# Kernel tuning notes

Hardware: AMD Instinct MI355X
Metric: run time of the kernel (lower is better)

The kernel has to match this reference:

```python
import jax, jax.numpy as jnp
import numpy as np

CDIM = 256  # part_size for energy_pooling_mask


def setup_inputs() -> dict:
    key = jax.random.key(0)
    ks = jax.random.split(key, 6)
    B, T, IDIM, HDIM, ODIM = 8, 2048, 512, 2048, 512
    x = jax.random.normal(ks[0], (B, T, IDIM), dtype=jnp.float32)
    mask_prev = jax.random.randint(ks[1], (B, T, HDIM), 0, 2, dtype=jnp.int32)
    W_enc = jax.random.normal(ks[2], (HDIM, IDIM), dtype=jnp.float32) * 0.02
    b_enc = jax.random.normal(ks[3], (HDIM,), dtype=jnp.float32) * 0.02
    W_dec = jax.random.normal(ks[4], (ODIM, HDIM), dtype=jnp.float32) * 0.02
    b_dec = jax.random.normal(ks[5], (ODIM,), dtype=jnp.float32) * 0.02
    return {"x": x, "mask_prev": mask_prev, "W_enc": W_enc, "b_enc": b_enc,
            "W_dec": W_dec, "b_dec": b_dec}


def _energy_pooling_mask(h, part_size):
    # topk over channel (last) dim of h^2; share=True -> k = 2*part_size
    B, T, H = h.shape
    k2 = 2 * part_size
    _, idx = jax.lax.top_k(h * h, k2)            # [B, T, 2c] unique indices
    idx_f = idx.reshape(B * T, k2)
    rows = jnp.arange(B * T)[:, None]
    base = jnp.zeros((B * T, H), dtype=h.dtype)
    # sum of one-hots over unique indices == scatter-set of 1.0
    mask_share = base.at[rows, idx_f].set(1.0).reshape(B, T, H)
    mask_cur = base.at[rows, idx_f[:, :part_size]].set(1.0).reshape(B, T, H)
    return mask_cur, mask_share


def reference(x, mask_prev, W_enc, b_enc, W_dec, b_dec):
    # encoder: Linear(idim -> hdim)
    h = jnp.einsum('bti,hi->bth', x, W_enc) + b_enc
    # hidden_exclude_activation with mask_prev given:
    # h[mask_prev.bool()] = 0
    mp = mask_prev.astype(h.dtype)
    h = jnp.where(mp > 0, jnp.zeros((), h.dtype), h)
    mask_cur, mask_cur_share = _energy_pooling_mask(h, CDIM)
    mask_prev_new = mp + mask_cur
    # h.masked_fill(~mask_cur_share.bool(), 0)
    h = h * mask_cur_share
    # decoder_src: Linear(hdim -> odim)
    out = jnp.einsum('bth,oh->bto', h, W_dec) + b_dec
    return out, mask_prev_new
```

## Files before the change

### kernel.cpp

```cpp
#include <hip/hip_runtime.h>
#include <hip/hip_bf16.h>

typedef __attribute__((ext_vector_type(8))) __bf16 bf16x8;
typedef __attribute__((ext_vector_type(4))) float f32x4;

#define MDIM 16384
#define HDIM 2048
#define IDIM 512
#define ODIM 512
#define CAP 768

static __device__ __forceinline__ unsigned short f2bf(float f) {
  unsigned int u = __float_as_uint(f);
  unsigned int r = (u + 0x7fffu + ((u >> 16) & 1u)) >> 16;
  return (unsigned short)r;
}

__global__ void cvt_bf16_kernel(const float* __restrict__ src,
                                unsigned short* __restrict__ dst, int n) {
  int i = (blockIdx.x * 256 + threadIdx.x) * 4;
  if (i >= n) return;
  float4 v = *(const float4*)(src + i);
  unsigned int a = (unsigned int)f2bf(v.x) | ((unsigned int)f2bf(v.y) << 16);
  unsigned int b = (unsigned int)f2bf(v.z) | ((unsigned int)f2bf(v.w) << 16);
  uint2 st; st.x = a; st.y = b;
  *(uint2*)(dst + i) = st;
}

__global__ __launch_bounds__(256) void gemm1_kernel(
    const float* __restrict__ x,
    const float* __restrict__ wenc,
    const float* __restrict__ benc,
    float* __restrict__ h,
    int m_base) {
  __shared__ __align__(16) float As[32][132];
  __shared__ __align__(16) float Bs[32][132];
  const int t = threadIdx.x;
  const int tx = t & 15, ty = t >> 4;
  const int m0 = m_base + blockIdx.y * 128;
  const int n0 = blockIdx.x * 128;
  const int r0 = t >> 1;
  const int kh = (t & 1) * 16;

  const float* pa = x + (size_t)(m0 + r0) * IDIM + kh;
  const float* pb = wenc + (size_t)(n0 + r0) * IDIM + kh;

  float acc[8][8];
#pragma unroll
  for (int i = 0; i < 8; ++i)
#pragma unroll
    for (int j = 0; j < 8; ++j) acc[i][j] = 0.f;

  for (int kt = 0; kt < IDIM; kt += 32) {
    float4 a0 = *(const float4*)(pa + kt);
    float4 a1 = *(const float4*)(pa + kt + 4);
    float4 a2 = *(const float4*)(pa + kt + 8);
    float4 a3 = *(const float4*)(pa + kt + 12);
    float4 b0 = *(const float4*)(pb + kt);
    float4 b1 = *(const float4*)(pb + kt + 4);
    float4 b2 = *(const float4*)(pb + kt + 8);
    float4 b3 = *(const float4*)(pb + kt + 12);
    __syncthreads();
    {
      const float av[16] = {a0.x, a0.y, a0.z, a0.w, a1.x, a1.y, a1.z, a1.w,
                            a2.x, a2.y, a2.z, a2.w, a3.x, a3.y, a3.z, a3.w};
      const float bv[16] = {b0.x, b0.y, b0.z, b0.w, b1.x, b1.y, b1.z, b1.w,
                            b2.x, b2.y, b2.z, b2.w, b3.x, b3.y, b3.z, b3.w};
#pragma unroll
      for (int j = 0; j < 16; ++j) {
        As[kh + j][r0] = av[j];
        Bs[kh + j][r0] = bv[j];
      }
    }
    __syncthreads();
#pragma unroll
    for (int k = 0; k < 32; ++k) {
      float4 av0 = *(const float4*)&As[k][ty * 4];
      float4 av1 = *(const float4*)&As[k][64 + ty * 4];
      float4 bv0 = *(const float4*)&Bs[k][tx * 4];
      float4 bv1 = *(const float4*)&Bs[k][64 + tx * 4];
      float am[8] = {av0.x, av0.y, av0.z, av0.w, av1.x, av1.y, av1.z, av1.w};
      float bm[8] = {bv0.x, bv0.y, bv0.z, bv0.w, bv1.x, bv1.y, bv1.z, bv1.w};
#pragma unroll
      for (int i = 0; i < 8; ++i)
#pragma unroll
        for (int j = 0; j < 8; ++j) acc[i][j] += am[i] * bm[j];
    }
  }
  float4 be0 = *(const float4*)(benc + n0 + tx * 4);
  float4 be1 = *(const float4*)(benc + n0 + 64 + tx * 4);
  float bb[8] = {be0.x, be0.y, be0.z, be0.w, be1.x, be1.y, be1.z, be1.w};
#pragma unroll
  for (int i = 0; i < 8; ++i) {
    int m = m0 + ((i < 4) ? (ty * 4 + i) : (64 + ty * 4 + (i - 4)));
    float* hrow = h + (size_t)m * HDIM + n0;
    float4 s0 = {acc[i][0] + bb[0], acc[i][1] + bb[1], acc[i][2] + bb[2], acc[i][3] + bb[3]};
    float4 s1 = {acc[i][4] + bb[4], acc[i][5] + bb[5], acc[i][6] + bb[6], acc[i][7] + bb[7]};
    *(float4*)(hrow + tx * 4) = s0;
    *(float4*)(hrow + 64 + tx * 4) = s1;
  }
}

__global__ __launch_bounds__(256) void select_kernel(
    float* __restrict__ hbuf,
    const int* __restrict__ maskp,
    unsigned short* __restrict__ hs) {
  const int row = blockIdx.x;
  const int t = threadIdx.x;
  const int lane = t & 63;
  const int w = t >> 6;
  __shared__ int hist[4096];
  __shared__ unsigned int cand512[CAP];
  __shared__ unsigned int cand256[CAP];
  __shared__ int scal[16];
  __shared__ int n512, n256;

  float* hrow = hbuf + (size_t)row * HDIM;
  const int* mrow = maskp + (size_t)row * HDIM;
  float hv[8];
  *(float4*)&hv[0] = *(const float4*)(hrow + t * 8);
  *(float4*)&hv[4] = *(const float4*)(hrow + t * 8 + 4);
  int4 mp0 = *(const int4*)(mrow + t * 8);
  int4 mp1 = *(const int4*)(mrow + t * 8 + 4);
  int mm[8] = {mp0.x, mp0.y, mp0.z, mp0.w, mp1.x, mp1.y, mp1.z, mp1.w};
#pragma unroll
  for (int i = 0; i < 8; ++i) hv[i] = (mm[i] > 0) ? 0.f : hv[i];
  unsigned int key[8];
#pragma unroll
  for (int i = 0; i < 8; ++i) key[i] = __float_as_uint(hv[i] * hv[i]);

#pragma unroll
  for (int i = 0; i < 16; ++i) hist[t + i * 256] = 0;
  if (t == 0) {
    n512 = 0; n256 = 0;
    scal[0] = 0; scal[1] = 0x40000000;
    scal[2] = 0; scal[3] = 0x40000000;
  }
  __syncthreads();
#pragma unroll
  for (int i = 0; i < 8; ++i)
    if (key[i]) atomicAdd(&hist[key[i] >> 20], 1);
  __syncthreads();

  if (w == 0) {
    const int base = lane * 64;
    int s = 0;
#pragma unroll
    for (int i = 0; i < 64; i += 4) {
      int4 hh = *(const int4*)&hist[base + i];
      s += hh.x + hh.y + hh.z + hh.w;
    }
    int rs = s;
#pragma unroll
    for (int d = 1; d < 64; d <<= 1) {
      int o = __shfl_down(rs, d, 64);
      rs += (lane + d < 64) ? o : 0;
    }
    int c = rs - s;
    for (int i = 60; i >= 0; i -= 4) {
      int4 hh = *(const int4*)&hist[base + i];
      int q[4] = {hh.x, hh.y, hh.z, hh.w};
#pragma unroll
      for (int j = 3; j >= 0; --j) {
        int hc = q[j];
        if (c < 512 && c + hc >= 512) { scal[0] = base + i + j; scal[1] = 512 - c; }
        if (c < 256 && c + hc >= 256) { scal[2] = base + i + j; scal[3] = 256 - c; }
        c += hc;
      }
    }
  }
  __syncthreads();
  const int b512 = scal[0], b256 = scal[2];
#pragma unroll
  for (int i = 0; i < 8; ++i) {
    if (key[i]) {
      int bin = (int)(key[i] >> 20);
      if (bin == b512) { int p = atomicAdd(&n512, 1); if (p < CAP) cand512[p] = key[i]; }
      if (bin == b256) { int p = atomicAdd(&n256, 1); if (p < CAP) cand256[p] = key[i]; }
    }
  }
  __syncthreads();

  if (w < 2) {
    const unsigned int bb = (unsigned int)scal[w * 2];
    const int r = scal[w * 2 + 1];
    const unsigned int* cand = w ? cand256 : cand512;
    int C = w ? n256 : n512;
    C = (C < CAP) ? C : CAP;
    unsigned int v = 0;
    if (r <= C) {
      v = bb << 20;
      for (int bit = 19; bit >= 0; --bit) {
        unsigned int cth = v | (1u << bit);
        int cnt = 0;
        for (int p = lane; p < C; p += 64) cnt += (cand[p] >= cth) ? 1 : 0;
#pragma unroll
        for (int d = 1; d < 64; d <<= 1) cnt += __shfl_xor(cnt, d, 64);
        if (cnt >= r) v = cth;
      }
    }
    if (lane == 0) scal[4 + w] = (int)v;
  }
  __syncthreads();
  const unsigned int v512 = (unsigned int)scal[4];
  const unsigned int v256 = (unsigned int)scal[5];

  int g = 0;
#pragma unroll
  for (int i = 0; i < 8; ++i) {
    g += (key[i] > v512) ? 1 : 0;
    g += (key[i] > v256) ? (1 << 16) : 0;
  }
#pragma unroll
  for (int d = 1; d < 64; d <<= 1) g += __shfl_xor(g, d, 64);
  if (lane == 0) scal[8 + w] = g;
  __syncthreads();
  g = scal[8] + scal[9] + scal[10] + scal[11];
  const int r512 = 512 - (g & 0xffff);
  const int r256 = 256 - (g >> 16);

  int tc = 0;
#pragma unroll
  for (int i = 0; i < 8; ++i) {
    tc += (key[i] == v512) ? 1 : 0;
    tc += (key[i] == v256) ? (1 << 16) : 0;
  }
  int sc = tc;
#pragma unroll
  for (int d = 1; d < 64; d <<= 1) {
    int o = __shfl_up(sc, d, 64);
    if (lane >= d) sc += o;
  }
  if (lane == 63) scal[12 + w] = sc;
  __syncthreads();
  int excl = sc - tc;
  for (int i = 0; i < w; ++i) excl += scal[12 + i];
  int run512 = excl & 0xffff;
  int run256 = (excl >> 16) & 0xffff;

  float mpn[8];
  unsigned int hb[4];
#pragma unroll
  for (int i = 0; i < 8; ++i) {
    bool share, cur;
    if (key[i] > v512) share = true;
    else if (key[i] == v512) { share = (run512 < r512); run512++; }
    else share = false;
    if (key[i] > v256) cur = true;
    else if (key[i] == v256) { cur = (run256 < r256); run256++; }
    else cur = false;
    mpn[i] = (float)mm[i] + (cur ? 1.0f : 0.0f);
    unsigned short bbits = f2bf(share ? hv[i] : 0.0f);
    if (i & 1) hb[i >> 1] |= ((unsigned int)bbits << 16);
    else hb[i >> 1] = (unsigned int)bbits;
  }
  float4 s0 = {mpn[0], mpn[1], mpn[2], mpn[3]};
  float4 s1 = {mpn[4], mpn[5], mpn[6], mpn[7]};
  *(float4*)(hrow + t * 8) = s0;
  *(float4*)(hrow + t * 8 + 4) = s1;
  uint4 hstore = {hb[0], hb[1], hb[2], hb[3]};
  *(uint4*)(hs + (size_t)row * HDIM + t * 8) = hstore;
}

__global__ __launch_bounds__(256) void gemm2_kernel(
    const unsigned short* __restrict__ A,
    const unsigned short* __restrict__ B,
    const float* __restrict__ bdec,
    float* __restrict__ out) {
  __shared__ __align__(16) unsigned short As[64 * 40];
  __shared__ __align__(16) unsigned short Bs[128 * 40];
  const int t = threadIdx.x;
  const int lane = t & 63;
  const int w = t >> 6;
  const int wm = w >> 1, wn = w & 1;
  const int m0 = blockIdx.y * 64;
  const int n0 = blockIdx.x * 128;
  const int r = t >> 2;
  const int k8 = (t & 3) * 8;

  f32x4 acc[2][4];
#pragma unroll
  for (int i = 0; i < 2; ++i)
#pragma unroll
    for (int j = 0; j < 4; ++j) acc[i][j] = (f32x4){0.f, 0.f, 0.f, 0.f};

  const int la = lane & 15;
  const int kq = (lane >> 4) * 8;

  for (int kt = 0; kt < HDIM; kt += 32) {
    uint4 a0 = *(const uint4*)(A + (size_t)(m0 + r) * HDIM + kt + k8);
    uint4 b0 = *(const uint4*)(B + (size_t)(n0 + r) * HDIM + kt + k8);
    uint4 b1 = *(const uint4*)(B + (size_t)(n0 + 64 + r) * HDIM + kt + k8);
    __syncthreads();
    *(uint4*)&As[r * 40 + k8] = a0;
    *(uint4*)&Bs[r * 40 + k8] = b0;
    *(uint4*)&Bs[(64 + r) * 40 + k8] = b1;
    __syncthreads();
    bf16x8 af[2], bg[4];
#pragma unroll
    for (int mi = 0; mi < 2; ++mi)
      af[mi] = *(const bf16x8*)&As[(wm * 32 + mi * 16 + la) * 40 + kq];
#pragma unroll
    for (int ni = 0; ni < 4; ++ni)
      bg[ni] = *(const bf16x8*)&Bs[(wn * 64 + ni * 16 + la) * 40 + kq];
#pragma unroll
    for (int mi = 0; mi < 2; ++mi)
#pragma unroll
      for (int ni = 0; ni < 4; ++ni)
        acc[mi][ni] = __builtin_amdgcn_mfma_f32_16x16x32_bf16(
            af[mi], bg[ni], acc[mi][ni], 0, 0, 0);
  }
  const int rq = (lane >> 4) * 4;
#pragma unroll
  for (int mi = 0; mi < 2; ++mi) {
#pragma unroll
    for (int ni = 0; ni < 4; ++ni) {
      int n = n0 + wn * 64 + ni * 16 + la;
      float bd = bdec[n];
#pragma unroll
      for (int rr = 0; rr < 4; ++rr) {
        int m = m0 + wm * 32 + mi * 16 + rq + rr;
        out[(size_t)m * ODIM + n] = acc[mi][ni][rr] + bd;
      }
    }
  }
}

extern "C" void kernel_launch(void* const* d_in, const int* in_sizes, int n_in,
                              void* d_out, int out_size, void* d_ws, size_t ws_size,
                              hipStream_t stream) {
  const float* x = (const float*)d_in[0];
  const int* mask_prev = (const int*)d_in[1];
  const float* W_enc = (const float*)d_in[2];
  const float* b_enc = (const float*)d_in[3];
  const float* W_dec = (const float*)d_in[4];
  const float* b_dec = (const float*)d_in[5];

  float* out = (float*)d_out;
  float* hbuf = out + (size_t)MDIM * ODIM;
  unsigned short* hs = (unsigned short*)d_ws;
  unsigned short* wdec = hs + (size_t)MDIM * HDIM;

  cvt_bf16_kernel<<<dim3((ODIM * HDIM) / (256 * 4)), dim3(256), 0, stream>>>(
      W_dec, wdec, ODIM * HDIM);
  for (int c = 0; c < 4; ++c) {
    gemm1_kernel<<<dim3(HDIM / 128, MDIM / 4 / 128), dim3(256), 0, stream>>>(
        x, W_enc, b_enc, hbuf, c * (MDIM / 4));
  }
  select_kernel<<<dim3(MDIM), dim3(256), 0, stream>>>(hbuf, mask_prev, hs);
  gemm2_kernel<<<dim3(ODIM / 128, MDIM / 64), dim3(256), 0, stream>>>(
      hs, wdec, b_dec, out);
}
```

Measured before the change: 884.0 us.

## Process one row per wavefront in select kernel to remove block barriers

```diff
diff --git a/kernel.cpp b/kernel.cpp
--- a/kernel.cpp
+++ b/kernel.cpp
@@ -8,7 +8,7 @@
 #define HDIM 2048
 #define IDIM 512
 #define ODIM 512
-#define CAP 768
+#define SCAP 512
 
 static __device__ __forceinline__ unsigned short f2bf(float f) {
   unsigned int u = __float_as_uint(f);
@@ -101,165 +101,191 @@
   }
 }
 
-__global__ __launch_bounds__(256) void select_kernel(
+__global__ __launch_bounds__(256, 4) void select_kernel(
     float* __restrict__ hbuf,
     const int* __restrict__ maskp,
     unsigned short* __restrict__ hs) {
-  const int row = blockIdx.x;
   const int t = threadIdx.x;
   const int lane = t & 63;
   const int w = t >> 6;
-  __shared__ int hist[4096];
-  __shared__ unsigned int cand512[CAP];
-  __shared__ unsigned int cand256[CAP];
-  __shared__ int scal[16];
-  __shared__ int n512, n256;
-
+  const int row = blockIdx.x * 4 + w;
+
+  __shared__ int hist[4][1024];
+  __shared__ unsigned int cand[4][2][SCAP];
+  __shared__ int nc[4][2];
+
+  int* H = hist[w];
   float* hrow = hbuf + (size_t)row * HDIM;
   const int* mrow = maskp + (size_t)row * HDIM;
-  float hv[8];
-  *(float4*)&hv[0] = *(const float4*)(hrow + t * 8);
-  *(float4*)&hv[4] = *(const float4*)(hrow + t * 8 + 4);
-  int4 mp0 = *(const int4*)(mrow + t * 8);
-  int4 mp1 = *(const int4*)(mrow + t * 8 + 4);
-  int mm[8] = {mp0.x, mp0.y, mp0.z, mp0.w, mp1.x, mp1.y, mp1.z, mp1.w};
-#pragma unroll
-  for (int i = 0; i < 8; ++i) hv[i] = (mm[i] > 0) ? 0.f : hv[i];
-  unsigned int key[8];
-#pragma unroll
-  for (int i = 0; i < 8; ++i) key[i] = __float_as_uint(hv[i] * hv[i]);
-
-#pragma unroll
-  for (int i = 0; i < 16; ++i) hist[t + i * 256] = 0;
-  if (t == 0) {
-    n512 = 0; n256 = 0;
-    scal[0] = 0; scal[1] = 0x40000000;
-    scal[2] = 0; scal[3] = 0x40000000;
-  }
-  __syncthreads();
-#pragma unroll
-  for (int i = 0; i < 8; ++i)
-    if (key[i]) atomicAdd(&hist[key[i] >> 20], 1);
-  __syncthreads();
-
-  if (w == 0) {
-    const int base = lane * 64;
-    int s = 0;
-#pragma unroll
-    for (int i = 0; i < 64; i += 4) {
-      int4 hh = *(const int4*)&hist[base + i];
-      s += hh.x + hh.y + hh.z + hh.w;
-    }
-    int rs = s;
+  unsigned short* hsrow = hs + (size_t)row * HDIM;
+
+  {
+    int4 z = {0, 0, 0, 0};
+#pragma unroll
+    for (int i = 0; i < 4; ++i) *(int4*)&H[(i * 64 + lane) * 4] = z;
+  }
+  if (lane == 0) { nc[w][0] = 0; nc[w][1] = 0; }
+
+  unsigned int key[8][4];
+  uint2 hvb[8];
+  unsigned int mmbits = 0;
+#pragma unroll
+  for (int s = 0; s < 8; ++s) {
+    float4 hv = *(const float4*)(hrow + (s * 64 + lane) * 4);
+    int4 mv = *(const int4*)(mrow + (s * 64 + lane) * 4);
+    float h0 = (mv.x > 0) ? 0.f : hv.x;
+    float h1 = (mv.y > 0) ? 0.f : hv.y;
+    float h2 = (mv.z > 0) ? 0.f : hv.z;
+    float h3 = (mv.w > 0) ? 0.f : hv.w;
+    mmbits |= ((mv.x > 0) ? 1u : 0u) << (s * 4 + 0);
+    mmbits |= ((mv.y > 0) ? 1u : 0u) << (s * 4 + 1);
+    mmbits |= ((mv.z > 0) ? 1u : 0u) << (s * 4 + 2);
+    mmbits |= ((mv.w > 0) ? 1u : 0u) << (s * 4 + 3);
+    key[s][0] = __float_as_uint(h0 * h0);
+    key[s][1] = __float_as_uint(h1 * h1);
+    key[s][2] = __float_as_uint(h2 * h2);
+    key[s][3] = __float_as_uint(h3 * h3);
+    hvb[s].x = (unsigned int)f2bf(h0) | ((unsigned int)f2bf(h1) << 16);
+    hvb[s].y = (unsigned int)f2bf(h2) | ((unsigned int)f2bf(h3) << 16);
+  }
+
+#pragma unroll
+  for (int s = 0; s < 8; ++s)
+#pragma unroll
+    for (int c = 0; c < 4; ++c)
+      if (key[s][c]) atomicAdd(&H[key[s][c] >> 21], 1);
+
+  int q[16];
+#pragma unroll
+  for (int i = 0; i < 16; i += 4) {
+    int4 hh = *(const int4*)&H[lane * 16 + i];
+    q[i] = hh.x; q[i + 1] = hh.y; q[i + 2] = hh.z; q[i + 3] = hh.w;
+  }
+  int ls = 0;
+#pragma unroll
+  for (int i = 0; i < 16; ++i) ls += q[i];
+  int rs = ls;
+#pragma unroll
+  for (int d = 1; d < 64; d <<= 1) {
+    int o = __shfl_down(rs, d, 64);
+    rs += (lane + d < 64) ? o : 0;
+  }
+  int f512 = -1, f256 = -1;
+  {
+    int c = rs - ls;
+#pragma unroll
+    for (int i = 15; i >= 0; --i) {
+      int hc = q[i];
+      if (c < 512 && c + hc >= 512) f512 = ((lane * 16 + i) << 12) | (512 - c);
+      if (c < 256 && c + hc >= 256) f256 = ((lane * 16 + i) << 12) | (256 - c);
+      c += hc;
+    }
+  }
+#pragma unroll
+  for (int d = 1; d < 64; d <<= 1) {
+    f512 = max(f512, __shfl_xor(f512, d, 64));
+    f256 = max(f256, __shfl_xor(f256, d, 64));
+  }
+  int b512, rb512, b256, rb256;
+  if (f512 < 0) { b512 = 0; rb512 = 0x40000000; } else { b512 = f512 >> 12; rb512 = f512 & 0xfff; }
+  if (f256 < 0) { b256 = 0; rb256 = 0x40000000; } else { b256 = f256 >> 12; rb256 = f256 & 0xfff; }
+
+  unsigned int* c5 = cand[w][0];
+  unsigned int* c2 = cand[w][1];
+#pragma unroll
+  for (int s = 0; s < 8; ++s)
+#pragma unroll
+    for (int c = 0; c < 4; ++c) {
+      unsigned int k = key[s][c];
+      if (k) {
+        int bin = (int)(k >> 21);
+        if (bin == b512) { int p = atomicAdd(&nc[w][0], 1); if (p < SCAP) c5[p] = k; }
+        if (bin == b256) { int p = atomicAdd(&nc[w][1], 1); if (p < SCAP) c2[p] = k; }
+      }
+    }
+  int C5 = nc[w][0]; C5 = (C5 < SCAP) ? C5 : SCAP;
+  int C2 = nc[w][1]; C2 = (C2 < SCAP) ? C2 : SCAP;
+
+  const int half = lane >> 5;
+  const int hl = lane & 31;
+  unsigned int bb = half ? (unsigned int)b256 : (unsigned int)b512;
+  int rr = half ? rb256 : rb512;
+  const unsigned int* cd = half ? c2 : c5;
+  int C = half ? C2 : C5;
+  unsigned int v = 0;
+  if (rr <= C) {
+    v = bb << 21;
+    for (int bit = 20; bit >= 0; --bit) {
+      unsigned int cth = v | (1u << bit);
+      int cnt = 0;
+      for (int p = hl; p < C; p += 32) cnt += (cd[p] >= cth) ? 1 : 0;
+#pragma unroll
+      for (int d = 1; d < 32; d <<= 1) cnt += __shfl_xor(cnt, d, 64);
+      if (cnt >= rr) v = cth;
+    }
+  }
+  const unsigned int v512 = (unsigned int)__shfl((int)v, 0, 64);
+  const unsigned int v256 = (unsigned int)__shfl((int)v, 32, 64);
+
+  int g = 0;
+#pragma unroll
+  for (int s = 0; s < 8; ++s)
+#pragma unroll
+    for (int c = 0; c < 4; ++c) {
+      g += (key[s][c] > v512) ? 1 : 0;
+      g += (key[s][c] > v256) ? (1 << 16) : 0;
+    }
+#pragma unroll
+  for (int d = 1; d < 64; d <<= 1) g += __shfl_xor(g, d, 64);
+  const int rg512 = 512 - (g & 0xffff);
+  const int rg256 = 256 - (g >> 16);
+
+  int excl = 0;
+#pragma unroll
+  for (int s = 0; s < 8; ++s) {
+    int tcnt = 0;
+#pragma unroll
+    for (int c = 0; c < 4; ++c) {
+      tcnt += (key[s][c] == v512) ? 1 : 0;
+      tcnt += (key[s][c] == v256) ? (1 << 16) : 0;
+    }
+    int incl = tcnt;
 #pragma unroll
     for (int d = 1; d < 64; d <<= 1) {
-      int o = __shfl_down(rs, d, 64);
-      rs += (lane + d < 64) ? o : 0;
-    }
-    int c = rs - s;
-    for (int i = 60; i >= 0; i -= 4) {
-      int4 hh = *(const int4*)&hist[base + i];
-      int q[4] = {hh.x, hh.y, hh.z, hh.w};
-#pragma unroll
-      for (int j = 3; j >= 0; --j) {
-        int hc = q[j];
-        if (c < 512 && c + hc >= 512) { scal[0] = base + i + j; scal[1] = 512 - c; }
-        if (c < 256 && c + hc >= 256) { scal[2] = base + i + j; scal[3] = 256 - c; }
-        c += hc;
+      int o = __shfl_up(incl, d, 64);
+      if (lane >= d) incl += o;
+    }
+    int myexcl = excl + incl - tcnt;
+    int tot = __shfl(incl, 63, 64);
+    int run512 = myexcl & 0xffff;
+    int run256 = (myexcl >> 16) & 0xffff;
+    float mpn[4];
+    unsigned int hb0 = hvb[s].x, hb1 = hvb[s].y;
+#pragma unroll
+    for (int c = 0; c < 4; ++c) {
+      unsigned int k = key[s][c];
+      bool share, cur;
+      if (k > v512) share = true;
+      else if (k == v512) { share = (run512 < rg512); run512++; }
+      else share = false;
+      if (k > v256) cur = true;
+      else if (k == v256) { cur = (run256 < rg256); run256++; }
+      else cur = false;
+      int mm = (mmbits >> (s * 4 + c)) & 1;
+      mpn[c] = (float)mm + (cur ? 1.0f : 0.0f);
+      if (!share) {
+        if (c == 0) hb0 &= 0xffff0000u;
+        if (c == 1) hb0 &= 0x0000ffffu;
+        if (c == 2) hb1 &= 0xffff0000u;
+        if (c == 3) hb1 &= 0x0000ffffu;
       }
     }
-  }
-  __syncthreads();
-  const int b512 = scal[0], b256 = scal[2];
-#pragma unroll
-  for (int i = 0; i < 8; ++i) {
-    if (key[i]) {
-      int bin = (int)(key[i] >> 20);
-      if (bin == b512) { int p = atomicAdd(&n512, 1); if (p < CAP) cand512[p] = key[i]; }
-      if (bin == b256) { int p = atomicAdd(&n256, 1); if (p < CAP) cand256[p] = key[i]; }
-    }
-  }
-  __syncthreads();
-
-  if (w < 2) {
-    const unsigned int bb = (unsigned int)scal[w * 2];
-    const int r = scal[w * 2 + 1];
-    const unsigned int* cand = w ? cand256 : cand512;
-    int C = w ? n256 : n512;
-    C = (C < CAP) ? C : CAP;
-    unsigned int v = 0;
-    if (r <= C) {
-      v = bb << 20;
-      for (int bit = 19; bit >= 0; --bit) {
-        unsigned int cth = v | (1u << bit);
-        int cnt = 0;
-        for (int p = lane; p < C; p += 64) cnt += (cand[p] >= cth) ? 1 : 0;
-#pragma unroll
-        for (int d = 1; d < 64; d <<= 1) cnt += __shfl_xor(cnt, d, 64);
-        if (cnt >= r) v = cth;
-      }
-    }
-    if (lane == 0) scal[4 + w] = (int)v;
-  }
-  __syncthreads();
-  const unsigned int v512 = (unsigned int)scal[4];
-  const unsigned int v256 = (unsigned int)scal[5];
-
-  int g = 0;
-#pragma unroll
-  for (int i = 0; i < 8; ++i) {
-    g += (key[i] > v512) ? 1 : 0;
-    g += (key[i] > v256) ? (1 << 16) : 0;
-  }
-#pragma unroll
-  for (int d = 1; d < 64; d <<= 1) g += __shfl_xor(g, d, 64);
-  if (lane == 0) scal[8 + w] = g;
-  __syncthreads();
-  g = scal[8] + scal[9] + scal[10] + scal[11];
-  const int r512 = 512 - (g & 0xffff);
-  const int r256 = 256 - (g >> 16);
-
-  int tc = 0;
-#pragma unroll
-  for (int i = 0; i < 8; ++i) {
-    tc += (key[i] == v512) ? 1 : 0;
-    tc += (key[i] == v256) ? (1 << 16) : 0;
-  }
-  int sc = tc;
-#pragma unroll
-  for (int d = 1; d < 64; d <<= 1) {
-    int o = __shfl_up(sc, d, 64);
-    if (lane >= d) sc += o;
-  }
-  if (lane == 63) scal[12 + w] = sc;
-  __syncthreads();
-  int excl = sc - tc;
-  for (int i = 0; i < w; ++i) excl += scal[12 + i];
-  int run512 = excl & 0xffff;
-  int run256 = (excl >> 16) & 0xffff;
-
-  float mpn[8];
-  unsigned int hb[4];
-#pragma unroll
-  for (int i = 0; i < 8; ++i) {
-    bool share, cur;
-    if (key[i] > v512) share = true;
-    else if (key[i] == v512) { share = (run512 < r512); run512++; }
-    else share = false;
-    if (key[i] > v256) cur = true;
-    else if (key[i] == v256) { cur = (run256 < r256); run256++; }
-    else cur = false;
-    mpn[i] = (float)mm[i] + (cur ? 1.0f : 0.0f);
-    unsigned short bbits = f2bf(share ? hv[i] : 0.0f);
-    if (i & 1) hb[i >> 1] |= ((unsigned int)bbits << 16);
-    else hb[i >> 1] = (unsigned int)bbits;
-  }
-  float4 s0 = {mpn[0], mpn[1], mpn[2], mpn[3]};
-  float4 s1 = {mpn[4], mpn[5], mpn[6], mpn[7]};
-  *(float4*)(hrow + t * 8) = s0;
-  *(float4*)(hrow + t * 8 + 4) = s1;
-  uint4 hstore = {hb[0], hb[1], hb[2], hb[3]};
-  *(uint4*)(hs + (size_t)row * HDIM + t * 8) = hstore;
+    float4 so = {mpn[0], mpn[1], mpn[2], mpn[3]};
+    *(float4*)(hrow + (s * 64 + lane) * 4) = so;
+    uint2 ho = {hb0, hb1};
+    *(uint2*)(hsrow + (s * 64 + lane) * 4) = ho;
+    excl += tot;
+  }
 }
 
 __global__ __launch_bounds__(256) void gemm2_kernel(
@@ -347,7 +373,7 @@
     gemm1_kernel<<<dim3(HDIM / 128, MDIM / 4 / 128), dim3(256), 0, stream>>>(
         x, W_enc, b_enc, hbuf, c * (MDIM / 4));
   }
-  select_kernel<<<dim3(MDIM), dim3(256), 0, stream>>>(hbuf, mask_prev, hs);
+  select_kernel<<<dim3(MDIM / 4), dim3(256), 0, stream>>>(hbuf, mask_prev, hs);
   gemm2_kernel<<<dim3(ODIM / 128, MDIM / 64), dim3(256), 0, stream>>>(
       hs, wdec, b_dec, out);
 }
```

New measurement: 801.1 us. 1.1x faster.
